# Kernel tuning notes

Measured on AMD Instinct MI355X. Metric: run time of the kernel, lower is better.

The kernel has to match this reference:

```python
import jax, jax.numpy as jnp
import numpy as np

B, D, G, S, K, E = 16384, 512, 8, 64, 64, 8  # batch, d_model, gate_len, select_embed_len, kernel_number, expert_num
H = 4 * S  # expert hidden width
EPS = 1e-5


def setup_inputs() -> dict:
    key = jax.random.key(0)
    ks = iter(jax.random.split(key, 40))

    def lin(kk, dout, din):
        return jax.random.normal(kk, (dout, din), jnp.float32) * (1.0 / np.sqrt(din))

    def bnp(n):
        g = 1.0 + 0.1 * jax.random.normal(next(ks), n, jnp.float32)  # gamma
        b = 0.1 * jax.random.normal(next(ks), n, jnp.float32)        # beta
        m = 0.1 * jax.random.normal(next(ks), n, jnp.float32)        # running_mean
        v = 1.0 + 0.5 * jax.random.uniform(next(ks), n, jnp.float32) # running_var
        return g, b, m, v

    inp = {"prompt": jax.random.normal(next(ks), (B, D), jnp.float32)}
    dims = [D, G * 8, G * 64, G * 128, G * S]
    for i in range(4):
        inp[f"W{i+1}"] = lin(next(ks), dims[i + 1], dims[i])
        g, b, m, v = bnp((dims[i + 1],))
        inp[f"g{i+1}"], inp[f"b{i+1}"], inp[f"m{i+1}"], inp[f"v{i+1}"] = g, b, m, v
    inp["We1"] = jax.random.normal(next(ks), (E, H, S), jnp.float32) * (1.0 / np.sqrt(S))
    inp["We2"] = jax.random.normal(next(ks), (E, K, H), jnp.float32) * (1.0 / np.sqrt(H))
    eg, eb, em, ev = bnp((E, G, H))
    inp["eg"], inp["eb"], inp["em"], inp["ev"] = eg, eb, em, ev
    return inp


def _lbr(x, W, g, b, m, v):
    # Linear(bias=False) -> BatchNorm1d (eval mode) -> ReLU
    h = x @ W.T
    return jax.nn.relu((h - m) * jax.lax.rsqrt(v + EPS) * g + b)


def reference(prompt, W1, g1, b1, m1, v1, W2, g2, b2, m2, v2,
              W3, g3, b3, m3, v3, W4, g4, b4, m4, v4,
              We1, We2, eg, eb, em, ev):
    h = _lbr(prompt, W1, g1, b1, m1, v1)
    h = _lbr(h, W2, g2, b2, m2, v2)
    h = _lbr(h, W3, g3, b3, m3, v3)
    h = _lbr(h, W4, g4, b4, m4, v4)
    enc = h.reshape(-1, G, S)  # [B, G, S]

    # Only expert 0 reaches the output in the original forward (selection[0]).
    x = jnp.einsum('bgs,hs->bgh', enc, We1[0])                        # [B, G, H]
    x = jax.nn.relu((x - em[0]) * jax.lax.rsqrt(ev[0] + EPS) * eg[0] + eb[0])
    x = jnp.einsum('bgh,kh->bgk', x, We2[0])                          # [B, G, K]

    s = jax.nn.sigmoid(x)
    s = jnp.clip(1.2 * s - 0.1, 0.0, 1.0)
    hard = (s > 0.49999).astype(s.dtype)  # straight-through step
    return s + jax.lax.stop_gradient(hard - s)
```

## Files before the change

### kernel.cpp

```cpp
#include <hip/hip_runtime.h>
#include <cmath>

__device__ __forceinline__ float bn_relu32(float h, float g, float b, float m, float v) {
#pragma clang fp contract(off)
    float vp = v + 1e-5f;
    float sq = (float)sqrt((double)vp);
    float rs = (float)(1.0 / (double)sq);
    float t = ((h - m) * rs) * g + b;
    return fmaxf(t, 0.0f);
}

__device__ __forceinline__ float hard_gate(float x) {
#pragma clang fp contract(off)
    float e = (float)exp((double)(-x));
    float d = 1.0f + e;
    float sg = (float)(1.0 / (double)d);
    float s = 1.2f * sg - 0.1f;
    s = fminf(fmaxf(s, 0.0f), 1.0f);
    return (s > 0.49999f) ? 1.0f : 0.0f;
}

template<int BM, int BN, int TM, int TN>
__global__ __launch_bounds__(256, 4)
void gemm_lbr(const float* __restrict__ A, long lda,
              const float* __restrict__ W, long ldw,
              const float* __restrict__ Pg, const float* __restrict__ Pb,
              const float* __restrict__ Pm, const float* __restrict__ Pv,
              float* __restrict__ C, long ldc, int K)
{
    constexpr int BK = 16, PAD = 4, NT = 256;
    constexpr int NX = BN / TN;
    __shared__ float As[BK][BM + PAD];
    __shared__ float Bs[BK][BN + PAD];

    const int t = threadIdx.x;
    const long m0 = (long)blockIdx.y * BM;
    const int n0 = blockIdx.x * BN;
    const float* Ab = A + m0 * lda;
    const float* Wb = W + (long)n0 * ldw;

    const int tx = t % NX;
    const int ty = t / NX;

    float acc[TM][TN];
#pragma unroll
    for (int i = 0; i < TM; ++i)
#pragma unroll
        for (int j = 0; j < TN; ++j) acc[i][j] = 0.0f;

    for (int k0 = 0; k0 < K; k0 += BK) {
#pragma unroll
        for (int i = 0; i < (BM * BK) / (4 * NT); ++i) {
            int idx = t + i * NT;
            int m = idx >> 2, kq = (idx & 3) << 2;
            float4 v = *reinterpret_cast<const float4*>(Ab + m * lda + k0 + kq);
            As[kq + 0][m] = v.x; As[kq + 1][m] = v.y;
            As[kq + 2][m] = v.z; As[kq + 3][m] = v.w;
        }
#pragma unroll
        for (int i = 0; i < (BN * BK) / (4 * NT); ++i) {
            int idx = t + i * NT;
            int n = idx >> 2, kq = (idx & 3) << 2;
            float4 v = *reinterpret_cast<const float4*>(Wb + n * ldw + k0 + kq);
            Bs[kq + 0][n] = v.x; Bs[kq + 1][n] = v.y;
            Bs[kq + 2][n] = v.z; Bs[kq + 3][n] = v.w;
        }
        __syncthreads();

#pragma unroll
        for (int kk = 0; kk < BK; ++kk) {
            float a[TM], b[TN];
#pragma unroll
            for (int i = 0; i < TM; i += 4)
                *reinterpret_cast<float4*>(&a[i]) =
                    *reinterpret_cast<const float4*>(&As[kk][ty * TM + i]);
            *reinterpret_cast<float4*>(&b[0]) =
                *reinterpret_cast<const float4*>(&Bs[kk][tx * 4]);
            if constexpr (TN == 8)
                *reinterpret_cast<float4*>(&b[4]) =
                    *reinterpret_cast<const float4*>(&Bs[kk][BN / 2 + tx * 4]);
#pragma unroll
            for (int i = 0; i < TM; ++i)
#pragma unroll
                for (int j = 0; j < TN; ++j)
                    acc[i][j] = fmaf(a[i], b[j], acc[i][j]);
        }
        __syncthreads();
    }

    const long crow = m0 + ty * TM;
#pragma unroll
    for (int h = 0; h < TN / 4; ++h) {
        int nbase = n0 + h * (BN / 2) + tx * 4;
        float gg[4], bb[4], mm[4], vv[4];
#pragma unroll
        for (int j = 0; j < 4; ++j) {
            gg[j] = Pg[nbase + j]; bb[j] = Pb[nbase + j];
            mm[j] = Pm[nbase + j]; vv[j] = Pv[nbase + j];
        }
#pragma unroll
        for (int i = 0; i < TM; ++i) {
            float4 o;
            o.x = bn_relu32(acc[i][h * 4 + 0], gg[0], bb[0], mm[0], vv[0]);
            o.y = bn_relu32(acc[i][h * 4 + 1], gg[1], bb[1], mm[1], vv[1]);
            o.z = bn_relu32(acc[i][h * 4 + 2], gg[2], bb[2], mm[2], vv[2]);
            o.w = bn_relu32(acc[i][h * 4 + 3], gg[3], bb[3], mm[3], vv[3]);
            *reinterpret_cast<float4*>(C + (crow + i) * ldc + nbase) = o;
        }
    }
}

#define B5 32
__global__ __launch_bounds__(256, 4)
void expert_fused(const float* __restrict__ h4,
                  const float* __restrict__ We1, const float* __restrict__ We2,
                  const float* __restrict__ eg, const float* __restrict__ eb,
                  const float* __restrict__ em, const float* __restrict__ ev,
                  float* __restrict__ out)
{
    __shared__ float As5[64][B5 + 4];
    __shared__ float xs[256][B5 + 4];
    __shared__ float Bs[16][256 + 4];

    const int t = threadIdx.x;
    const long m0 = (long)blockIdx.x * B5;
    const int g = blockIdx.y;

#pragma unroll
    for (int it = 0; it < 2; ++it) {
        int idx4 = t + it * 256;
        int m = idx4 >> 4, sq = (idx4 & 15) << 2;
        float4 v = *reinterpret_cast<const float4*>(h4 + (m0 + m) * 512 + g * 64 + sq);
        As5[sq + 0][m] = v.x; As5[sq + 1][m] = v.y;
        As5[sq + 2][m] = v.z; As5[sq + 3][m] = v.w;
    }

    const int tx = t & 31, ty = t >> 5;
    float acc5[4][8];
#pragma unroll
    for (int i = 0; i < 4; ++i)
#pragma unroll
        for (int j = 0; j < 8; ++j) acc5[i][j] = 0.0f;

    for (int k0 = 0; k0 < 64; k0 += 16) {
        __syncthreads();
#pragma unroll
        for (int it = 0; it < 4; ++it) {
            int idx4 = t + it * 256;
            int hh = idx4 >> 2, kq = (idx4 & 3) << 2;
            float4 v = *reinterpret_cast<const float4*>(We1 + hh * 64 + k0 + kq);
            Bs[kq + 0][hh] = v.x; Bs[kq + 1][hh] = v.y;
            Bs[kq + 2][hh] = v.z; Bs[kq + 3][hh] = v.w;
        }
        __syncthreads();
#pragma unroll
        for (int kk = 0; kk < 16; ++kk) {
            float a[4];
            *reinterpret_cast<float4*>(a) =
                *reinterpret_cast<const float4*>(&As5[k0 + kk][ty * 4]);
            float b[8];
#pragma unroll
            for (int c = 0; c < 4; ++c)
                *reinterpret_cast<float2*>(&b[c * 2]) =
                    *reinterpret_cast<const float2*>(&Bs[kk][tx * 2 + c * 64]);
#pragma unroll
            for (int i = 0; i < 4; ++i)
#pragma unroll
                for (int j = 0; j < 8; ++j)
                    acc5[i][j] = fmaf(a[i], b[j], acc5[i][j]);
        }
    }
    __syncthreads();

#pragma unroll
    for (int c = 0; c < 4; ++c)
#pragma unroll
        for (int u = 0; u < 2; ++u) {
            int hh = tx * 2 + c * 64 + u;
            long p = (long)g * 256 + hh;
            float gg = eg[p], bb = eb[p], mm = em[p], vv = ev[p];
#pragma unroll
            for (int i = 0; i < 4; ++i)
                xs[hh][ty * 4 + i] = bn_relu32(acc5[i][c * 2 + u], gg, bb, mm, vv);
        }

    float acc6[4][2];
#pragma unroll
    for (int i = 0; i < 4; ++i) { acc6[i][0] = 0.0f; acc6[i][1] = 0.0f; }

    for (int k0 = 0; k0 < 256; k0 += 16) {
        __syncthreads();
        {
            int kk = t >> 2, khq = (t & 3) << 2;
            float4 v = *reinterpret_cast<const float4*>(We2 + kk * 256 + k0 + khq);
            Bs[khq + 0][kk] = v.x; Bs[khq + 1][kk] = v.y;
            Bs[khq + 2][kk] = v.z; Bs[khq + 3][kk] = v.w;
        }
        __syncthreads();
#pragma unroll
        for (int kh = 0; kh < 16; ++kh) {
            float a[4];
            *reinterpret_cast<float4*>(a) =
                *reinterpret_cast<const float4*>(&xs[k0 + kh][ty * 4]);
            float2 b = *reinterpret_cast<const float2*>(&Bs[kh][tx * 2]);
#pragma unroll
            for (int i = 0; i < 4; ++i) {
                acc6[i][0] = fmaf(a[i], b.x, acc6[i][0]);
                acc6[i][1] = fmaf(a[i], b.y, acc6[i][1]);
            }
        }
    }

#pragma unroll
    for (int i = 0; i < 4; ++i) {
        float2 o;
        o.x = hard_gate(acc6[i][0]);
        o.y = hard_gate(acc6[i][1]);
        *reinterpret_cast<float2*>(out + (m0 + ty * 4 + i) * 512 + g * 64 + tx * 2) = o;
    }
}

#define FNT 512
template<int CPT, int RPT, int EPI>
__device__ __forceinline__ void flayer(
    const float* __restrict__ I, int ldI, int K,
    const float* __restrict__ Wt, long ldW,
    const float* __restrict__ Pg, const float* __restrict__ Pb,
    const float* __restrict__ Pm, const float* __restrict__ Pv,
    float* __restrict__ O, int ldO, int n, int r0, int rstep)
{
    float acc[CPT][RPT];
#pragma unroll
    for (int c = 0; c < CPT; ++c)
#pragma unroll
        for (int r = 0; r < RPT; ++r) acc[c][r] = 0.0f;
#pragma unroll 2
    for (int k = 0; k < K; k += 4) {
        float4 av[RPT];
#pragma unroll
        for (int r = 0; r < RPT; ++r)
            av[r] = *reinterpret_cast<const float4*>(I + (r0 + r * rstep) * ldI + k);
#pragma unroll
        for (int c = 0; c < CPT; ++c) {
            float4 w = *reinterpret_cast<const float4*>(Wt + (long)(n + c * FNT) * ldW + k);
#pragma unroll
            for (int r = 0; r < RPT; ++r) {
                acc[c][r] = fmaf(av[r].x, w.x, acc[c][r]);
                acc[c][r] = fmaf(av[r].y, w.y, acc[c][r]);
                acc[c][r] = fmaf(av[r].z, w.z, acc[c][r]);
                acc[c][r] = fmaf(av[r].w, w.w, acc[c][r]);
            }
        }
    }
#pragma unroll
    for (int c = 0; c < CPT; ++c) {
        int nn = n + c * FNT;
        if constexpr (EPI == 1) {
            float gg = Pg[nn], bb = Pb[nn], mm = Pm[nn], vv = Pv[nn];
#pragma unroll
            for (int r = 0; r < RPT; ++r)
                O[(r0 + r * rstep) * ldO + nn] = bn_relu32(acc[c][r], gg, bb, mm, vv);
        } else {
#pragma unroll
            for (int r = 0; r < RPT; ++r)
                O[(r0 + r * rstep) * ldO + nn] = hard_gate(acc[c][r]);
        }
    }
}

__global__ __launch_bounds__(FNT, 4)
void tg32_fused(const float* __restrict__ prompt,
    const float* __restrict__ W1, const float* __restrict__ g1, const float* __restrict__ b1, const float* __restrict__ m1, const float* __restrict__ v1,
    const float* __restrict__ W2, const float* __restrict__ g2, const float* __restrict__ b2, const float* __restrict__ m2, const float* __restrict__ v2,
    const float* __restrict__ W3, const float* __restrict__ g3, const float* __restrict__ b3, const float* __restrict__ m3, const float* __restrict__ v3,
    const float* __restrict__ W4, const float* __restrict__ g4, const float* __restrict__ b4, const float* __restrict__ m4, const float* __restrict__ v4,
    const float* __restrict__ We1, const float* __restrict__ We2,
    const float* __restrict__ eg, const float* __restrict__ eb, const float* __restrict__ em, const float* __restrict__ ev,
    float* __restrict__ out)
{
    __shared__ __align__(16) float arena[12288];
    float* A0 = arena;
    float* A1 = arena + 4096;
    const int t = threadIdx.x;
    const long row0 = (long)blockIdx.x * 8;
    for (int i = t; i < 1024; i += FNT) {
        int r = i >> 7, c4 = (i & 127) << 2;
        *reinterpret_cast<float4*>(A0 + r * 512 + c4) =
            *reinterpret_cast<const float4*>(prompt + (row0 + r) * 512 + c4);
    }
    __syncthreads();
    flayer<1, 1, 1>(A0, 512, 512, W1, 512, g1, b1, m1, v1, A1, 64, t & 63, t >> 6, 1);
    __syncthreads();
    flayer<1, 8, 1>(A1, 64, 64, W2, 64, g2, b2, m2, v2, A0, 512, t, 0, 1);
    __syncthreads();
    flayer<2, 8, 1>(A0, 512, 512, W3, 512, g3, b3, m3, v3, A1, 1024, t, 0, 1);
    __syncthreads();
    flayer<1, 8, 1>(A1, 1024, 1024, W4, 1024, g4, b4, m4, v4, A0, 512, t, 0, 1);
    __syncthreads();
    for (int g = 0; g < 8; ++g) {
        flayer<1, 4, 1>(A0 + g * 64, 512, 64, We1, 64,
                        eg + g * 256, eb + g * 256, em + g * 256, ev + g * 256,
                        A1, 256, t & 255, (t >> 8) * 4, 1);
        __syncthreads();
        flayer<1, 1, 2>(A1, 256, 256, We2, 256, nullptr, nullptr, nullptr, nullptr,
                        out + row0 * 512 + g * 64, 512, t & 63, t >> 6, 1);
        __syncthreads();
    }
}

extern "C" void kernel_launch(void* const* d_in, const int* in_sizes, int n_in,
                              void* d_out, int out_size, void* d_ws, size_t ws_size,
                              hipStream_t stream) {
    (void)n_in; (void)out_size;
    const float* prompt = (const float*)d_in[0];
    const float* W1 = (const float*)d_in[1];
    const float* g1 = (const float*)d_in[2];
    const float* b1 = (const float*)d_in[3];
    const float* m1 = (const float*)d_in[4];
    const float* v1 = (const float*)d_in[5];
    const float* W2 = (const float*)d_in[6];
    const float* g2 = (const float*)d_in[7];
    const float* b2 = (const float*)d_in[8];
    const float* m2 = (const float*)d_in[9];
    const float* v2 = (const float*)d_in[10];
    const float* W3 = (const float*)d_in[11];
    const float* g3 = (const float*)d_in[12];
    const float* b3 = (const float*)d_in[13];
    const float* m3 = (const float*)d_in[14];
    const float* v3 = (const float*)d_in[15];
    const float* W4 = (const float*)d_in[16];
    const float* g4 = (const float*)d_in[17];
    const float* b4 = (const float*)d_in[18];
    const float* m4 = (const float*)d_in[19];
    const float* v4 = (const float*)d_in[20];
    const float* We1 = (const float*)d_in[21];
    const float* We2 = (const float*)d_in[22];
    const float* eg = (const float*)d_in[23];
    const float* eb = (const float*)d_in[24];
    const float* em = (const float*)d_in[25];
    const float* ev = (const float*)d_in[26];
    float* out = (float*)d_out;

    const long Btot = in_sizes[0] / 512;
    const long perRow = 2112;
    long Bc = (long)(ws_size / (perRow * 4));
    if (Bc > Btot) Bc = Btot;
    Bc &= ~127L;

    if (Bc < 128) {
        tg32_fused<<<dim3(Btot / 8), dim3(FNT), 0, stream>>>(prompt,
            W1, g1, b1, m1, v1, W2, g2, b2, m2, v2,
            W3, g3, b3, m3, v3, W4, g4, b4, m4, v4,
            We1, We2, eg, eb, em, ev, out);
        return;
    }

    float* h1 = (float*)d_ws;
    float* h2 = h1 + Bc * 64;
    float* h3 = h2 + Bc * 512;
    float* h4 = h3 + Bc * 1024;

    for (long b0 = 0; b0 < Btot; b0 += Bc) {
        long mc = Btot - b0; if (mc > Bc) mc = Bc;
        const float* P = prompt + b0 * 512;
        dim3 blk(256);
        gemm_lbr<64, 64, 4, 4><<<dim3(1, mc / 64), blk, 0, stream>>>(
            P, 512, W1, 512, g1, b1, m1, v1, h1, 64, 512);
        gemm_lbr<128, 128, 8, 8><<<dim3(4, mc / 128), blk, 0, stream>>>(
            h1, 64, W2, 64, g2, b2, m2, v2, h2, 512, 64);
        gemm_lbr<128, 128, 8, 8><<<dim3(8, mc / 128), blk, 0, stream>>>(
            h2, 512, W3, 512, g3, b3, m3, v3, h3, 1024, 512);
        gemm_lbr<128, 128, 8, 8><<<dim3(4, mc / 128), blk, 0, stream>>>(
            h3, 1024, W4, 1024, g4, b4, m4, v4, h4, 512, 1024);
        expert_fused<<<dim3(mc / 32, 8), blk, 0, stream>>>(
            h4, We1, We2, eg, eb, em, ev, out + b0 * 512);
    }
}
```

Baseline: 623.1 us.

## Prefetch next K tile into registers and double BK in LBR GEMM

The LBR GEMM kernel now loads the next K tile from global memory into registers while computing on the current shared-memory tile, then stores it to shared memory after a barrier. BK grows from 16 to 32, and the thread count and minimum occupancy become template parameters; layer 3 runs with 128 threads and a 16x8 per-thread tile. The goal is to hide global load latency and halve the barrier count, at the cost of more registers and shared memory and lower occupancy hints.

```diff
diff --git a/kernel.cpp b/kernel.cpp
--- a/kernel.cpp
+++ b/kernel.cpp
@@ -20,15 +20,17 @@
     return (s > 0.49999f) ? 1.0f : 0.0f;
 }
 
-template<int BM, int BN, int TM, int TN>
-__global__ __launch_bounds__(256, 4)
+template<int BM, int BN, int TM, int TN, int NT, int MINW>
+__global__ __launch_bounds__(NT, MINW)
 void gemm_lbr(const float* __restrict__ A, long lda,
               const float* __restrict__ W, long ldw,
               const float* __restrict__ Pg, const float* __restrict__ Pb,
               const float* __restrict__ Pm, const float* __restrict__ Pv,
               float* __restrict__ C, long ldc, int K)
 {
-    constexpr int BK = 16, PAD = 4, NT = 256;
+    constexpr int BK = 32, PAD = 4;
+    constexpr int LA = (BM * BK) / (4 * NT);
+    constexpr int LB = (BN * BK) / (4 * NT);
     constexpr int NX = BN / TN;
     __shared__ float As[BK][BM + PAD];
     __shared__ float Bs[BK][BN + PAD];
@@ -38,9 +40,40 @@
     const int n0 = blockIdx.x * BN;
     const float* Ab = A + m0 * lda;
     const float* Wb = W + (long)n0 * ldw;
-
-    const int tx = t % NX;
-    const int ty = t / NX;
+    const int tx = t % NX, ty = t / NX;
+
+    float4 ra[LA], rb[LB];
+
+    auto load_tile = [&](int k0) {
+#pragma unroll
+        for (int i = 0; i < LA; ++i) {
+            int idx = t + i * NT;
+            int m = idx >> 3, kq = (idx & 7) << 2;
+            ra[i] = *reinterpret_cast<const float4*>(Ab + m * lda + k0 + kq);
+        }
+#pragma unroll
+        for (int i = 0; i < LB; ++i) {
+            int idx = t + i * NT;
+            int n = idx >> 3, kq = (idx & 7) << 2;
+            rb[i] = *reinterpret_cast<const float4*>(Wb + n * ldw + k0 + kq);
+        }
+    };
+    auto store_tile = [&]() {
+#pragma unroll
+        for (int i = 0; i < LA; ++i) {
+            int idx = t + i * NT;
+            int m = idx >> 3, kq = (idx & 7) << 2;
+            As[kq + 0][m] = ra[i].x; As[kq + 1][m] = ra[i].y;
+            As[kq + 2][m] = ra[i].z; As[kq + 3][m] = ra[i].w;
+        }
+#pragma unroll
+        for (int i = 0; i < LB; ++i) {
+            int idx = t + i * NT;
+            int n = idx >> 3, kq = (idx & 7) << 2;
+            Bs[kq + 0][n] = rb[i].x; Bs[kq + 1][n] = rb[i].y;
+            Bs[kq + 2][n] = rb[i].z; Bs[kq + 3][n] = rb[i].w;
+        }
+    };
 
     float acc[TM][TN];
 #pragma unroll
@@ -48,44 +81,35 @@
 #pragma unroll
         for (int j = 0; j < TN; ++j) acc[i][j] = 0.0f;
 
-    for (int k0 = 0; k0 < K; k0 += BK) {
-#pragma unroll
-        for (int i = 0; i < (BM * BK) / (4 * NT); ++i) {
-            int idx = t + i * NT;
-            int m = idx >> 2, kq = (idx & 3) << 2;
-            float4 v = *reinterpret_cast<const float4*>(Ab + m * lda + k0 + kq);
-            As[kq + 0][m] = v.x; As[kq + 1][m] = v.y;
-            As[kq + 2][m] = v.z; As[kq + 3][m] = v.w;
-        }
-#pragma unroll
-        for (int i = 0; i < (BN * BK) / (4 * NT); ++i) {
-            int idx = t + i * NT;
-            int n = idx >> 2, kq = (idx & 3) << 2;
-            float4 v = *reinterpret_cast<const float4*>(Wb + n * ldw + k0 + kq);
-            Bs[kq + 0][n] = v.x; Bs[kq + 1][n] = v.y;
-            Bs[kq + 2][n] = v.z; Bs[kq + 3][n] = v.w;
-        }
-        __syncthreads();
-
-#pragma unroll
+    load_tile(0);
+    store_tile();
+    __syncthreads();
+
+    const int ntk = K / BK;
+    for (int kt = 0; kt < ntk; ++kt) {
+        if (kt + 1 < ntk) load_tile((kt + 1) * BK);
+#pragma unroll 8
         for (int kk = 0; kk < BK; ++kk) {
             float a[TM], b[TN];
 #pragma unroll
             for (int i = 0; i < TM; i += 4)
                 *reinterpret_cast<float4*>(&a[i]) =
                     *reinterpret_cast<const float4*>(&As[kk][ty * TM + i]);
-            *reinterpret_cast<float4*>(&b[0]) =
-                *reinterpret_cast<const float4*>(&Bs[kk][tx * 4]);
-            if constexpr (TN == 8)
-                *reinterpret_cast<float4*>(&b[4]) =
-                    *reinterpret_cast<const float4*>(&Bs[kk][BN / 2 + tx * 4]);
+#pragma unroll
+            for (int h = 0; h < TN / 4; ++h)
+                *reinterpret_cast<float4*>(&b[h * 4]) =
+                    *reinterpret_cast<const float4*>(&Bs[kk][h * (BN / 2) + tx * 4]);
 #pragma unroll
             for (int i = 0; i < TM; ++i)
 #pragma unroll
                 for (int j = 0; j < TN; ++j)
                     acc[i][j] = fmaf(a[i], b[j], acc[i][j]);
         }
-        __syncthreads();
+        if (kt + 1 < ntk) {
+            __syncthreads();
+            store_tile();
+            __syncthreads();
+        }
     }
 
     const long crow = m0 + ty * TM;
@@ -363,16 +387,15 @@
     for (long b0 = 0; b0 < Btot; b0 += Bc) {
         long mc = Btot - b0; if (mc > Bc) mc = Bc;
         const float* P = prompt + b0 * 512;
-        dim3 blk(256);
-        gemm_lbr<64, 64, 4, 4><<<dim3(1, mc / 64), blk, 0, stream>>>(
+        gemm_lbr<64, 64, 4, 4, 256, 3><<<dim3(1, mc / 64), dim3(256), 0, stream>>>(
             P, 512, W1, 512, g1, b1, m1, v1, h1, 64, 512);
-        gemm_lbr<128, 128, 8, 8><<<dim3(4, mc / 128), blk, 0, stream>>>(
+        gemm_lbr<128, 128, 8, 8, 256, 3><<<dim3(4, mc / 128), dim3(256), 0, stream>>>(
             h1, 64, W2, 64, g2, b2, m2, v2, h2, 512, 64);
-        gemm_lbr<128, 128, 8, 8><<<dim3(8, mc / 128), blk, 0, stream>>>(
+        gemm_lbr<128, 128, 16, 8, 128, 2><<<dim3(8, mc / 128), dim3(128), 0, stream>>>(
             h2, 512, W3, 512, g3, b3, m3, v3, h3, 1024, 512);
-        gemm_lbr<128, 128, 8, 8><<<dim3(4, mc / 128), blk, 0, stream>>>(
+        gemm_lbr<128, 128, 8, 8, 256, 3><<<dim3(4, mc / 128), dim3(256), 0, stream>>>(
             h3, 1024, W4, 1024, g4, b4, m4, v4, h4, 512, 1024);
-        expert_fused<<<dim3(mc / 32, 8), blk, 0, stream>>>(
+        expert_fused<<<dim3(mc / 32, 8), dim3(256), 0, stream>>>(
             h4, We1, We2, eg, eb, em, ev, out + b0 * 512);
     }
 }
```

Result: slower. 656.8 us (+5.4%).
